# Kernel tuning notes

Measured on AMD Instinct MI355X. Metric: run time of the kernel, lower is better.

The kernel has to match this reference:

```python
import jax, jax.numpy as jnp
import numpy as np
from jax import lax

BATCH = 8192
PATCH = 2
STRIDE = 2
OUT_CH = 4
NUM_PATCHES = ((28 - PATCH) // STRIDE + 1) ** 2  # 196
THRESHOLD = 0.8
EPS = 1e-12


def setup_inputs() -> dict:
    key = jax.random.key(0)
    k1, k2, k3, k4, k5 = jax.random.split(key, 5)
    x = jax.random.normal(k1, (BATCH, 1, 28, 28), dtype=jnp.float32)
    conv_w = jax.random.normal(k2, (OUT_CH, 1, PATCH, PATCH), dtype=jnp.float32) * 0.5
    conv_b = jax.random.normal(k3, (OUT_CH,), dtype=jnp.float32) * 0.1
    feat_dim = OUT_CH * NUM_PATCHES + NUM_PATCHES  # 784 + 196 = 980
    lin_w = jax.random.normal(k4, (10, feat_dim), dtype=jnp.float32) * 0.02
    lin_b = jax.random.normal(k5, (10,), dtype=jnp.float32) * 0.01
    return {"x": x, "conv_w": conv_w, "conv_b": conv_b, "lin_w": lin_w, "lin_b": lin_b}


def reference(x, conv_w, conv_b, lin_w, lin_b):
    # conv patch embed: (B,1,28,28) -> (B,C,14,14)
    f = lax.conv_general_dilated(
        x, conv_w, window_strides=(STRIDE, STRIDE), padding="VALID",
        dimension_numbers=("NCHW", "OIHW", "NCHW"))
    f = f + conv_b[None, :, None, None]
    B = f.shape[0]
    flat = f.reshape(B, -1)  # (B, C*P) channel-major, matches torch .view
    # replicate feat.view(num_patches, -1): rows of length C from the flat vector
    pf = flat.reshape(B, NUM_PATCHES, -1)  # (B, P, C)
    nrm = pf / (jnp.linalg.norm(pf, axis=-1, keepdims=True) + EPS)
    # squared cosine similarity = state fidelity, all pairs at once
    fid = jnp.einsum("bpc,bqc->bpq", nrm, nrm) ** 2  # (B, P, P)
    w = (fid >= THRESHOLD).astype(flat.dtype)
    w = w * (1.0 - jnp.eye(NUM_PATCHES, dtype=flat.dtype))  # no self-edges
    deg = jnp.sum(w, axis=-1)  # weighted degree per node, (B, P)
    feats = jnp.concatenate([flat, deg], axis=1)  # (B, 980)
    logits = feats @ lin_w.T + lin_b
    return jax.nn.log_softmax(logits, axis=-1)
```

## Files before the change

kernel.cpp:

```cpp
#include <hip/hip_runtime.h>
#include <math.h>


#define NP 196
#define FEAT 980
#define COS_TH 0.894427190999915878f

typedef float v2f __attribute__((ext_vector_type(2)));
typedef float v4f __attribute__((ext_vector_type(4)));

__global__ __launch_bounds__(256, 6) void quanv_kernel(
    const float* __restrict__ x,
    const float* __restrict__ conv_w,
    const float* __restrict__ conv_b,
    const float* __restrict__ lin_w,
    const float* __restrict__ lin_b,
    float* __restrict__ out)
{
    __shared__ __align__(16) float s_x[2][784];
    __shared__ __align__(16) float s_n[2][4][256];
    __shared__ __align__(16) float s_feats[2][FEAT];

    const int b = blockIdx.x;
    const int t = threadIdx.x;
    const int w = t >> 6, l = t & 63;

    if (t < NP) {
        ((float4*)s_x[0])[t] = ((const float4*)(x + (size_t)(2 * b)     * 784))[t];
        ((float4*)s_x[1])[t] = ((const float4*)(x + (size_t)(2 * b + 1) * 784))[t];
    }
    __syncthreads();

    if (t < NP) {
        int h = t / 14, ww = t - 14 * (t / 14);
        #pragma unroll
        for (int img = 0; img < 2; ++img) {
            const float* r0 = s_x[img] + (2 * h) * 28 + 2 * ww;
            float x00 = r0[0], x01 = r0[1], x10 = r0[28], x11 = r0[29];
            #pragma unroll
            for (int c = 0; c < 4; ++c) {
                float f = conv_b[c]
                        + conv_w[c * 4 + 0] * x00 + conv_w[c * 4 + 1] * x01
                        + conv_w[c * 4 + 2] * x10 + conv_w[c * 4 + 3] * x11;
                s_feats[img][c * NP + t] = f;
            }
        }
    }
    __syncthreads();

    #pragma unroll
    for (int img = 0; img < 2; ++img) {
        if (t < NP) {
            float4 v = ((const float4*)s_feats[img])[t];
            float n = sqrtf(v.x * v.x + v.y * v.y + v.z * v.z + v.w * v.w);
            float inv = 1.0f / (n + 1e-12f);
            s_n[img][0][t] = v.x * inv; s_n[img][1][t] = v.y * inv;
            s_n[img][2][t] = v.z * inv; s_n[img][3][t] = v.w * inv;
        } else {
            s_n[img][0][t] = 0.f; s_n[img][1][t] = 0.f;
            s_n[img][2][t] = 0.f; s_n[img][3][t] = 0.f;
        }
    }
    __syncthreads();

    #pragma unroll
    for (int img = 0; img < 2; ++img) {
        unsigned* s_cnt = (unsigned*)s_x[img];
        v2f mx[3], my[3], mz[3], mw[3];
        #pragma unroll
        for (int r = 0; r < 3; ++r) {
            int row = l + 64 * r;
            float px = s_n[img][0][row], py = s_n[img][1][row];
            float pz = s_n[img][2][row], pw = s_n[img][3][row];
            mx[r] = (v2f){px, px};
            my[r] = (v2f){py, py};
            mz[r] = (v2f){pz, pz};
            mw[r] = (v2f){pw, pw};
        }
        #pragma unroll
        for (int r = 0; r < 3; ++r)
            asm("" : "+v"(mx[r]), "+v"(my[r]), "+v"(mz[r]), "+v"(mw[r]));

        unsigned cnt[3] = {0u, 0u, 0u};
        const float* qb = &s_n[img][0][52 * w];
        #pragma unroll
        for (int j = 0; j < 13; ++j) {
            v4f qx = *(const v4f*)(qb + 4 * j);
            v4f qy = *(const v4f*)(qb + 256 + 4 * j);
            v4f qz = *(const v4f*)(qb + 512 + 4 * j);
            v4f qw = *(const v4f*)(qb + 768 + 4 * j);
            v2f qx0 = __builtin_shufflevector(qx, qx, 0, 1);
            v2f qx1 = __builtin_shufflevector(qx, qx, 2, 3);
            v2f qy0 = __builtin_shufflevector(qy, qy, 0, 1);
            v2f qy1 = __builtin_shufflevector(qy, qy, 2, 3);
            v2f qz0 = __builtin_shufflevector(qz, qz, 0, 1);
            v2f qz1 = __builtin_shufflevector(qz, qz, 2, 3);
            v2f qw0 = __builtin_shufflevector(qw, qw, 0, 1);
            v2f qw1 = __builtin_shufflevector(qw, qw, 2, 3);
            #pragma unroll
            for (int r = 0; r < 3; ++r) {
                v2f d0, d1;
                asm("v_pk_mul_f32 %0, %1, %2"     : "=v"(d0) : "v"(qx0), "v"(mx[r]));
                asm("v_pk_mul_f32 %0, %1, %2"     : "=v"(d1) : "v"(qx1), "v"(mx[r]));
                asm("v_pk_fma_f32 %0, %1, %2, %0" : "+v"(d0) : "v"(qy0), "v"(my[r]));
                asm("v_pk_fma_f32 %0, %1, %2, %0" : "+v"(d1) : "v"(qy1), "v"(my[r]));
                asm("v_pk_fma_f32 %0, %1, %2, %0" : "+v"(d0) : "v"(qz0), "v"(mz[r]));
                asm("v_pk_fma_f32 %0, %1, %2, %0" : "+v"(d1) : "v"(qz1), "v"(mz[r]));
                asm("v_pk_fma_f32 %0, %1, %2, %0" : "+v"(d0) : "v"(qw0), "v"(mw[r]));
                asm("v_pk_fma_f32 %0, %1, %2, %0" : "+v"(d1) : "v"(qw1), "v"(mw[r]));
                cnt[r] += (fabsf(d0.x) >= COS_TH);
                cnt[r] += (fabsf(d0.y) >= COS_TH);
                cnt[r] += (fabsf(d1.x) >= COS_TH);
                cnt[r] += (fabsf(d1.y) >= COS_TH);
            }
        }
        s_cnt[t] = cnt[0] | (cnt[1] << 8) | (cnt[2] << 16);

        int row = 192 + w;
        float px = s_n[img][0][row], py = s_n[img][1][row];
        float pz = s_n[img][2][row], pw = s_n[img][3][row];
        unsigned total = 0u;
        #pragma unroll
        for (int j = 0; j < 4; ++j) {
            int q = 64 * j + l;
            float d = px * s_n[img][0][q];
            d = fmaf(py, s_n[img][1][q], d);
            d = fmaf(pz, s_n[img][2][q], d);
            d = fmaf(pw, s_n[img][3][q], d);
            unsigned long long m = __ballot(fabsf(d) >= COS_TH);
            total += (unsigned)__popcll(m);
        }
        if (l == 0) s_feats[img][784 + row] = (float)(total - 1u);
    }
    __syncthreads();

    if (t < 192) {
        int c = t >> 6, ll = t & 63;
        #pragma unroll
        for (int img = 0; img < 2; ++img) {
            const unsigned* s_cnt = (const unsigned*)s_x[img];
            unsigned s = ((s_cnt[ll]       >> (8 * c)) & 255u)
                       + ((s_cnt[64 + ll]  >> (8 * c)) & 255u)
                       + ((s_cnt[128 + ll] >> (8 * c)) & 255u)
                       + ((s_cnt[192 + ll] >> (8 * c)) & 255u);
            s_feats[img][784 + t] = (float)(s - 1u);
        }
    }
    __syncthreads();

    if (t < 250) {
        int k = t / 25, c = t - 25 * (t / 25);
        const float4* wrow = (const float4*)(lin_w + k * FEAT);
        const float4* f0p = (const float4*)s_feats[0];
        const float4* f1p = (const float4*)s_feats[1];
        float a0 = 0.0f, a1 = 0.0f;
        for (int i = c; i < 245; i += 25) {
            float4 wv = wrow[i];
            float4 f0 = f0p[i];
            float4 f1 = f1p[i];
            a0 = fmaf(f0.x, wv.x, a0); a1 = fmaf(f1.x, wv.x, a1);
            a0 = fmaf(f0.y, wv.y, a0); a1 = fmaf(f1.y, wv.y, a1);
            a0 = fmaf(f0.z, wv.z, a0); a1 = fmaf(f1.z, wv.z, a1);
            a0 = fmaf(f0.w, wv.w, a0); a1 = fmaf(f1.w, wv.w, a1);
        }
        (s_x[0] + 256)[t] = a0;
        (s_x[1] + 256)[t] = a1;
    }
    __syncthreads();

    if (t < 20) {
        int img = t / 10, k = t - 10 * (t / 10);
        const float* part = s_x[img] + 256;
        float s = lin_b[k];
        #pragma unroll
        for (int i = 0; i < 25; ++i) s += part[k * 25 + i];
        (s_x[img] + 512)[k] = s;
    }
    __syncthreads();

    if (t < 20) {
        int img = t / 10, k = t - 10 * (t / 10);
        const float* lg = s_x[img] + 512;
        float m = -INFINITY;
        #pragma unroll
        for (int j = 0; j < 10; ++j) m = fmaxf(m, lg[j]);
        float s = 0.0f;
        #pragma unroll
        for (int j = 0; j < 10; ++j) s += expf(lg[j] - m);
        out[(size_t)(2 * b + img) * 10 + k] = lg[k] - m - logf(s);
    }
}

extern "C" void kernel_launch(void* const* d_in, const int* in_sizes, int n_in,
                              void* d_out, int out_size, void* d_ws, size_t ws_size,
                              hipStream_t stream) {
    const float* x      = (const float*)d_in[0];
    const float* conv_w = (const float*)d_in[1];
    const float* conv_b = (const float*)d_in[2];
    const float* lin_w  = (const float*)d_in[3];
    const float* lin_b  = (const float*)d_in[4];
    float* out = (float*)d_out;
    quanv_kernel<<<dim3(4096), dim3(256), 0, stream>>>(x, conv_w, conv_b, lin_w, lin_b, out);
}
```

Before: 120.5 us.

## Compute patch similarity matrix with bf16 split-precision MFMA instead of packed FP32

Replaces the packed-FP32 all-pairs dot product with 32x32x16 bf16 MFMA. Each normalized 4-vector is split into bf16 high and low parts so the product keeps near-FP32 accuracy, and the 14 column-tile jobs are spread over the four waves. The goal is to move the O(P^2) similarity work onto matrix cores and drop the separate tail-row ballot pass and the count-reduction stage. In exchange it adds bf16 rounding error near the threshold, which could flip edge counts, and it does 16x-padded MFMA work plus per-element compare loops.

```diff
diff --git a/kernel.cpp b/kernel.cpp
--- a/kernel.cpp
+++ b/kernel.cpp
@@ -6,8 +6,9 @@
 #define FEAT 980
 #define COS_TH 0.894427190999915878f
 
-typedef float v2f __attribute__((ext_vector_type(2)));
-typedef float v4f __attribute__((ext_vector_type(4)));
+typedef short v4s  __attribute__((ext_vector_type(4)));
+typedef short v8s  __attribute__((ext_vector_type(8)));
+typedef float v16f __attribute__((ext_vector_type(16)));
 
 __global__ __launch_bounds__(256, 6) void quanv_kernel(
     const float* __restrict__ x,
@@ -18,7 +19,7 @@
     float* __restrict__ out)
 {
     __shared__ __align__(16) float s_x[2][784];
-    __shared__ __align__(16) float s_n[2][4][256];
+    __shared__ __align__(16) short s_P[2][224][8];
     __shared__ __align__(16) float s_feats[2][FEAT];
 
     const int b = blockIdx.x;
@@ -48,102 +49,61 @@
     }
     __syncthreads();
 
-    #pragma unroll
-    for (int img = 0; img < 2; ++img) {
-        if (t < NP) {
-            float4 v = ((const float4*)s_feats[img])[t];
-            float n = sqrtf(v.x * v.x + v.y * v.y + v.z * v.z + v.w * v.w);
-            float inv = 1.0f / (n + 1e-12f);
-            s_n[img][0][t] = v.x * inv; s_n[img][1][t] = v.y * inv;
-            s_n[img][2][t] = v.z * inv; s_n[img][3][t] = v.w * inv;
-        } else {
-            s_n[img][0][t] = 0.f; s_n[img][1][t] = 0.f;
-            s_n[img][2][t] = 0.f; s_n[img][3][t] = 0.f;
+    if (t < 224) {
+        #pragma unroll
+        for (int img = 0; img < 2; ++img) {
+            v8s pk = {0, 0, 0, 0, 0, 0, 0, 0};
+            if (t < NP) {
+                float4 v = ((const float4*)s_feats[img])[t];
+                float n = sqrtf(v.x * v.x + v.y * v.y + v.z * v.z + v.w * v.w);
+                float inv = 1.0f / (n + 1e-12f);
+                float e[4] = { v.x * inv, v.y * inv, v.z * inv, v.w * inv };
+                #pragma unroll
+                for (int k = 0; k < 4; ++k) {
+                    uint32_t bx = __float_as_uint(e[k]);
+                    uint32_t rh = bx + 0x7FFFu + ((bx >> 16) & 1u);
+                    uint32_t hk = rh >> 16;
+                    float hif = __uint_as_float(hk << 16);
+                    float res = e[k] - hif;
+                    uint32_t br = __float_as_uint(res);
+                    uint32_t rl = br + 0x7FFFu + ((br >> 16) & 1u);
+                    pk[k]     = (short)hk;
+                    pk[4 + k] = (short)(rl >> 16);
+                }
+            }
+            *(v8s*)&s_P[img][t][0] = pk;
         }
     }
     __syncthreads();
 
-    #pragma unroll
-    for (int img = 0; img < 2; ++img) {
-        unsigned* s_cnt = (unsigned*)s_x[img];
-        v2f mx[3], my[3], mz[3], mw[3];
+    for (int job = w; job < 14; job += 4) {
+        const int img = (job >= 7) ? 1 : 0;
+        const int j = job - 7 * img;
+        const int ln = l & 31, half = l >> 5;
+
+        v4s bh = *(const v4s*)&s_P[img][32 * j + ln][4 * half];
+        v8s B = __builtin_shufflevector(bh, bh, 0, 1, 2, 3, 0, 1, 2, 3);
+
+        v8s A[7];
         #pragma unroll
-        for (int r = 0; r < 3; ++r) {
-            int row = l + 64 * r;
-            float px = s_n[img][0][row], py = s_n[img][1][row];
-            float pz = s_n[img][2][row], pw = s_n[img][3][row];
-            mx[r] = (v2f){px, px};
-            my[r] = (v2f){py, py};
-            mz[r] = (v2f){pz, pz};
-            mw[r] = (v2f){pw, pw};
+        for (int i = 0; i < 7; ++i)
+            A[i] = *(const v8s*)&s_P[img][32 * i + ln][0];
+
+        unsigned cnt = 0u;
+        #pragma unroll
+        for (int i = 0; i < 7; ++i) {
+            v16f acc = {0.f,0.f,0.f,0.f,0.f,0.f,0.f,0.f,
+                        0.f,0.f,0.f,0.f,0.f,0.f,0.f,0.f};
+            acc = __builtin_amdgcn_mfma_f32_32x32x16_bf16(A[i], B, acc, 0, 0, 0);
+            #pragma unroll
+            for (int e = 0; e < 16; ++e)
+                cnt += (fabsf(acc[e]) >= COS_TH) ? 1u : 0u;
         }
-        #pragma unroll
-        for (int r = 0; r < 3; ++r)
-            asm("" : "+v"(mx[r]), "+v"(my[r]), "+v"(mz[r]), "+v"(mw[r]));
-
-        unsigned cnt[3] = {0u, 0u, 0u};
-        const float* qb = &s_n[img][0][52 * w];
-        #pragma unroll
-        for (int j = 0; j < 13; ++j) {
-            v4f qx = *(const v4f*)(qb + 4 * j);
-            v4f qy = *(const v4f*)(qb + 256 + 4 * j);
-            v4f qz = *(const v4f*)(qb + 512 + 4 * j);
-            v4f qw = *(const v4f*)(qb + 768 + 4 * j);
-            v2f qx0 = __builtin_shufflevector(qx, qx, 0, 1);
-            v2f qx1 = __builtin_shufflevector(qx, qx, 2, 3);
-            v2f qy0 = __builtin_shufflevector(qy, qy, 0, 1);
-            v2f qy1 = __builtin_shufflevector(qy, qy, 2, 3);
-            v2f qz0 = __builtin_shufflevector(qz, qz, 0, 1);
-            v2f qz1 = __builtin_shufflevector(qz, qz, 2, 3);
-            v2f qw0 = __builtin_shufflevector(qw, qw, 0, 1);
-            v2f qw1 = __builtin_shufflevector(qw, qw, 2, 3);
-            #pragma unroll
-            for (int r = 0; r < 3; ++r) {
-                v2f d0, d1;
-                asm("v_pk_mul_f32 %0, %1, %2"     : "=v"(d0) : "v"(qx0), "v"(mx[r]));
-                asm("v_pk_mul_f32 %0, %1, %2"     : "=v"(d1) : "v"(qx1), "v"(mx[r]));
-                asm("v_pk_fma_f32 %0, %1, %2, %0" : "+v"(d0) : "v"(qy0), "v"(my[r]));
-                asm("v_pk_fma_f32 %0, %1, %2, %0" : "+v"(d1) : "v"(qy1), "v"(my[r]));
-                asm("v_pk_fma_f32 %0, %1, %2, %0" : "+v"(d0) : "v"(qz0), "v"(mz[r]));
-                asm("v_pk_fma_f32 %0, %1, %2, %0" : "+v"(d1) : "v"(qz1), "v"(mz[r]));
-                asm("v_pk_fma_f32 %0, %1, %2, %0" : "+v"(d0) : "v"(qw0), "v"(mw[r]));
-                asm("v_pk_fma_f32 %0, %1, %2, %0" : "+v"(d1) : "v"(qw1), "v"(mw[r]));
-                cnt[r] += (fabsf(d0.x) >= COS_TH);
-                cnt[r] += (fabsf(d0.y) >= COS_TH);
-                cnt[r] += (fabsf(d1.x) >= COS_TH);
-                cnt[r] += (fabsf(d1.y) >= COS_TH);
-            }
-        }
-        s_cnt[t] = cnt[0] | (cnt[1] << 8) | (cnt[2] << 16);
-
-        int row = 192 + w;
-        float px = s_n[img][0][row], py = s_n[img][1][row];
-        float pz = s_n[img][2][row], pw = s_n[img][3][row];
-        unsigned total = 0u;
-        #pragma unroll
-        for (int j = 0; j < 4; ++j) {
-            int q = 64 * j + l;
-            float d = px * s_n[img][0][q];
-            d = fmaf(py, s_n[img][1][q], d);
-            d = fmaf(pz, s_n[img][2][q], d);
-            d = fmaf(pw, s_n[img][3][q], d);
-            unsigned long long m = __ballot(fabsf(d) >= COS_TH);
-            total += (unsigned)__popcll(m);
-        }
-        if (l == 0) s_feats[img][784 + row] = (float)(total - 1u);
-    }
-    __syncthreads();
-
-    if (t < 192) {
-        int c = t >> 6, ll = t & 63;
-        #pragma unroll
-        for (int img = 0; img < 2; ++img) {
-            const unsigned* s_cnt = (const unsigned*)s_x[img];
-            unsigned s = ((s_cnt[ll]       >> (8 * c)) & 255u)
-                       + ((s_cnt[64 + ll]  >> (8 * c)) & 255u)
-                       + ((s_cnt[128 + ll] >> (8 * c)) & 255u)
-                       + ((s_cnt[192 + ll] >> (8 * c)) & 255u);
-            s_feats[img][784 + t] = (float)(s - 1u);
+        cnt += __shfl_down(cnt, 32, 64);
+        if (l < 32) {
+            int col = 32 * j + l;
+            if (col < NP)
+                s_feats[img][784 + col] = (float)(int)cnt - 1.0f;
         }
     }
     __syncthreads();
@@ -183,10 +143,10 @@
         const float* lg = s_x[img] + 512;
         float m = -INFINITY;
         #pragma unroll
-        for (int j = 0; j < 10; ++j) m = fmaxf(m, lg[j]);
+        for (int j2 = 0; j2 < 10; ++j2) m = fmaxf(m, lg[j2]);
         float s = 0.0f;
         #pragma unroll
-        for (int j = 0; j < 10; ++j) s += expf(lg[j] - m);
+        for (int j2 = 0; j2 < 10; ++j2) s += expf(lg[j2] - m);
         out[(size_t)(2 * b + img) * 10 + k] = lg[k] - m - logf(s);
     }
 }
```

Result: faster. 109.5 us (-9.1%).
